# Optimization experiments

Measured on AMD Instinct MI355X. Metric: run time of the kernel, lower is better.

Reference implementation:

```python
import jax, jax.numpy as jnp
import numpy as np

INF = 1e10  # stand-in for +inf boundary of soft-DTW DP (safe under exp(-INF/gamma)=0)
HUBER_DELTA = 1.0
SDTW_ALPHA = 0.1
SDTW_GAMMA = 0.1


def _softmin3(a, b, c, gamma):
    # soft-min_gamma(a,b,c) = -gamma * logsumexp(-a/g, -b/g, -c/g)
    s = jnp.stack([a, b, c], axis=0) * (-1.0 / gamma)
    return -gamma * jax.nn.logsumexp(s, axis=0)


def _soft_dtw(x, y, gamma):
    # x, y: (B, L, C). Returns per-batch soft-DTW value R[L-1, L-1], shape (B,).
    B, L, C = x.shape
    # pairwise squared-euclidean distances (B, L, L) without (B,L,L,C) blowup
    x2 = jnp.sum(x * x, axis=-1)  # (B, L)
    y2 = jnp.sum(y * y, axis=-1)  # (B, L)
    D = x2[:, :, None] + y2[:, None, :] - 2.0 * jnp.einsum('blc,bmc->blm', x, y)

    i = jnp.arange(L)

    # Diagonals are stored as (B, L+1) arrays indexed by p = i + 1, so that the
    # virtual cell R[-1,-1] = 0 lives at p = 0 of diagonal k = -2.
    def step(carry, k):
        r2, r1 = carry  # diagonals k-2 and k-1
        j = k - i
        valid = (j >= 0) & (j < L)
        jc = jnp.clip(j, 0, L - 1)
        d = jnp.take_along_axis(D, jc[None, :, None], axis=2)[:, :, 0]  # (B, L) = D[:, i, k-i]
        a = r2[:, :-1]  # R[i-1, j-1]
        b = r1[:, :-1]  # R[i-1, j]
        c = r1[:, 1:]   # R[i, j-1]
        rk_vals = jnp.where(valid[None, :], d + _softmin3(a, b, c, gamma), INF)
        rk = jnp.concatenate([jnp.full((B, 1), INF, D.dtype), rk_vals], axis=1)
        return (r1, rk), None

    r2 = jnp.full((B, L + 1), INF, D.dtype).at[:, 0].set(0.0)  # diag k=-2: R[-1,-1]=0
    r1 = jnp.full((B, L + 1), INF, D.dtype)                    # diag k=-1: all inf
    (_, rlast), _ = jax.lax.scan(step, (r2, r1), jnp.arange(2 * L - 1))
    return rlast[:, L]  # R[L-1, L-1] per batch


def _huber_mean(x_hat, x, delta):
    d = x_hat - x
    ad = jnp.abs(d)
    loss = jnp.where(ad <= delta, 0.5 * d * d, delta * (ad - 0.5 * delta))
    return jnp.mean(loss)


def setup_inputs() -> dict:
    key = jax.random.key(0)
    k1, k2, k3 = jax.random.split(key, 3)
    B, L, C = 64, 512, 16
    x = jax.random.normal(k1, (B, L, C), dtype=jnp.float32)
    x_hat = jax.random.normal(k2, (B, L, C), dtype=jnp.float32)
    commitment_loss = jax.random.uniform(k3, (), dtype=jnp.float32)
    return {"x": x, "x_hat": x_hat, "commitment_loss": commitment_loss}


def reference(x, x_hat, commitment_loss):
    huber = _huber_mean(x_hat, x, HUBER_DELTA)
    sdtw = jnp.mean(_soft_dtw(x, x_hat, SDTW_GAMMA)) * SDTW_ALPHA
    total = huber + sdtw + commitment_loss
    # stacked [total, huber, sdtw, commitment] (torch module returns a dict of these scalars)
    return jnp.stack([total, huber, sdtw, commitment_loss])
```

## Files before the change

kernel.cpp:

```cpp
#include <hip/hip_runtime.h>
#include <math.h>


#define INFV 1.0e10f
static constexpr float kC1 = 14.4269504088896f;
static constexpr float kC2 = 0.0693147180559945f;

__device__ __forceinline__ int diag_off(int k) {
  if (k <= 512) return (k * (k + 1)) >> 1;
  int u = k - 512;
  return 131328 + 511 * u - ((u * (u - 1)) >> 1);
}
__device__ __forceinline__ int diag_i0(int k) { return k < 512 ? 0 : k - 511; }

__device__ __forceinline__ float huber1(float d) {
  float ad = fabsf(d);
  return ad <= 1.0f ? 0.5f * d * d : ad - 0.5f;
}

__global__ __launch_bounds__(256) void huber_kernel(const float* __restrict__ x,
                                                    const float* __restrict__ xh,
                                                    float* __restrict__ part) {
  int t = threadIdx.x;
  int gid = blockIdx.x * 256 + t;
  float s = 0.f;
  for (int i = gid; i < 131072; i += 65536) {
    float4 a = ((const float4*)x)[i];
    float4 b = ((const float4*)xh)[i];
    s += huber1(b.x - a.x) + huber1(b.y - a.y) + huber1(b.z - a.z) + huber1(b.w - a.w);
  }
  for (int o = 32; o > 0; o >>= 1) s += __shfl_down(s, o, 64);
  __shared__ float ws4[4];
  if ((t & 63) == 0) ws4[t >> 6] = s;
  __syncthreads();
  if (t == 0) part[blockIdx.x] = ws4[0] + ws4[1] + ws4[2] + ws4[3];
}

__global__ __launch_bounds__(256) void gemm_diag_kernel(const float* __restrict__ x,
                                                        const float* __restrict__ xh,
                                                        float* __restrict__ Dp) {
  const int b = blockIdx.z;
  const int ti = blockIdx.x;
  const int tj = blockIdx.y;
  const int t = threadIdx.x;
  __shared__ float sm[64 * 67];
  float* xsT = sm;
  float* ysT = sm + 16 * 68;
  const float* xb = x + ((size_t)b * 8192) + ti * 1024;
  const float* yb = xh + ((size_t)b * 8192) + tj * 1024;
  {
    float4 xv = ((const float4*)xb)[t];
    float4 yv = ((const float4*)yb)[t];
    int r = t >> 2, c0 = (t & 3) << 2;
    xsT[(c0 + 0) * 68 + r] = xv.x;
    xsT[(c0 + 1) * 68 + r] = xv.y;
    xsT[(c0 + 2) * 68 + r] = xv.z;
    xsT[(c0 + 3) * 68 + r] = xv.w;
    ysT[(c0 + 0) * 68 + r] = yv.x;
    ysT[(c0 + 1) * 68 + r] = yv.y;
    ysT[(c0 + 2) * 68 + r] = yv.z;
    ysT[(c0 + 3) * 68 + r] = yv.w;
  }
  __syncthreads();
  const int tm = t & 15, tn = t >> 4;
  float acc[4][4] = {};
  float y2a[4] = {};
#pragma unroll
  for (int c = 0; c < 16; ++c) {
    float4 xv = *(const float4*)&xsT[c * 68 + tm * 4];
    float4 yv = *(const float4*)&ysT[c * 68 + tn * 4];
    float xr[4] = {xv.x, xv.y, xv.z, xv.w};
    float yr[4] = {yv.x, yv.y, yv.z, yv.w};
#pragma unroll
    for (int n = 0; n < 4; ++n) {
      y2a[n] = fmaf(yr[n], yr[n], y2a[n]);
#pragma unroll
      for (int m = 0; m < 4; ++m) acc[m][n] = fmaf(xr[m], yr[n], acc[m][n]);
    }
  }
  __syncthreads();
#pragma unroll
  for (int m = 0; m < 4; ++m)
#pragma unroll
    for (int n = 0; n < 4; ++n)
      sm[(tm * 4 + m) * 67 + (tn * 4 + n)] = acc[m][n] - 0.5f * y2a[n];
  __syncthreads();
  const int lane = t & 63, wv = t >> 6;
  float* outb = Dp + (size_t)b * 262144;
  const int kbase = ti * 64 + tj * 64;
  for (int s = wv; s < 127; s += 4) {
    int ilo = s > 63 ? s - 63 : 0;
    int ihi = s < 63 ? s : 63;
    if (lane >= ilo && lane <= ihi) {
      float v = sm[lane * 67 + (s - lane)];
      int k = kbase + s;
      outb[diag_off(k) - diag_i0(k) + (ti * 64 + lane)] = v;
    }
  }
}

#define PSTEP(PN)                                                           \
  do {                                                                      \
    float bval = __shfl_up(vprev, 1);                                       \
    float rv = ringPrev[min(kk + 63, 574)];                                 \
    if (lane == 0) bval = (w == 0) ? INFV : rv;                             \
    float mv = fminf(fminf(aval, bval), vprev);                             \
    float md = __builtin_amdgcn_fmed3f(aval, bval, vprev);                  \
    float mx = fmaxf(fmaxf(aval, bval), vprev);                             \
    float ssum = 1.0f + exp2f((mv - md) * kC1) + exp2f((mv - mx) * kC1);    \
    float sm3 = fmaf(-kC2, log2f(ssum), mv);                                \
    float dotv = PN;                                                        \
    {                                                                       \
      int kc = k0 + min(kk + 10, 574);                                      \
      PN = DbL[diag_off(kc) - diag_i0(kc)];                                 \
    }                                                                       \
    float dd = fmaf(-2.0f, dotv, x2);                                       \
    float val = ((unsigned)(kk - lane) <= 511u) ? (dd + sm3) : INFV;        \
    if (lane == 63) ringOwn[kk] = val;                                      \
    aval = bval;                                                            \
    vprev = val;                                                            \
    ++kk;                                                                   \
  } while (0)

__global__ __launch_bounds__(512) void dtw_pipe_kernel(const float* __restrict__ x,
                                                       const float* __restrict__ Dp,
                                                       float* __restrict__ outv) {
  const int b = blockIdx.x;
  const int tid = threadIdx.x;
  const int w = tid >> 6;
  const int lane = tid & 63;
  __shared__ float ring[8][576];
  __shared__ int flags[8];
  if (tid < 8) flags[tid] = 0;
  __syncthreads();
  volatile int* vflags = flags;

  const int i = (w << 6) | lane;
  const float* xr = x + (size_t)b * 8192 + i * 16;
  float x2 = 0.f;
#pragma unroll
  for (int c = 0; c < 16; c += 4) {
    float4 v = *(const float4*)(xr + c);
    x2 += v.x * v.x + v.y * v.y + v.z * v.z + v.w * v.w;
  }
  const float* DbL = Dp + (size_t)b * 262144 + i;
  const int k0 = w << 6;

  float p[10];
#pragma unroll
  for (int n = 0; n < 10; ++n) {
    int kg = k0 + n;
    p[n] = DbL[diag_off(kg) - diag_i0(kg)];
  }

  float aval = (w == 0 && lane == 0) ? 0.0f : INFV;
  float vprev = INFV;
  float* ringOwn = ring[w];
  const float* ringPrev = ring[(w == 0) ? 7 : (w - 1)];

  int kk = 0;
#pragma unroll 1
  for (int ss = 0; ss < 58; ++ss) {
    const int nsub = (ss == 57) ? 5 : 10;
    if (w != 0) {
      const int need = min(kk + nsub + 63, 575);
      while (vflags[w - 1] < need) {
      }
      __threadfence_block();
    }
    if (nsub == 10) {
      PSTEP(p[0]); PSTEP(p[1]); PSTEP(p[2]); PSTEP(p[3]); PSTEP(p[4]);
      PSTEP(p[5]); PSTEP(p[6]); PSTEP(p[7]); PSTEP(p[8]); PSTEP(p[9]);
    } else {
      PSTEP(p[0]); PSTEP(p[1]); PSTEP(p[2]); PSTEP(p[3]); PSTEP(p[4]);
    }
    __threadfence_block();
    if (lane == 63) vflags[w] = kk;
  }
  if (tid == 511) outv[b] = vprev;
}

__device__ __forceinline__ float dot16(const float4& a, const float4& b2,
                                       const float4& c, const float4& d,
                                       const float4* yp) {
  float4 q0 = yp[0], q1 = yp[1], q2 = yp[2], q3 = yp[3];
  float s = a.x * q0.x;
  s = fmaf(a.y, q0.y, s); s = fmaf(a.z, q0.z, s); s = fmaf(a.w, q0.w, s);
  s = fmaf(b2.x, q1.x, s); s = fmaf(b2.y, q1.y, s); s = fmaf(b2.z, q1.z, s); s = fmaf(b2.w, q1.w, s);
  s = fmaf(c.x, q2.x, s); s = fmaf(c.y, q2.y, s); s = fmaf(c.w, q2.w, s); s = fmaf(c.z, q2.z, s);
  s = fmaf(d.x, q3.x, s); s = fmaf(d.y, q3.y, s); s = fmaf(d.z, q3.z, s); s = fmaf(d.w, q3.w, s);
  return s;
}

#define DTW_FSTEP(W, R1, R2)                                                \
  do {                                                                      \
    int j = k - tid;                                                        \
    bool valid = (j >= 0) && (j < 512);                                     \
    int jc = valid ? j : 0;                                                 \
    float av = R2[tid];                                                     \
    float bv = R1[tid];                                                     \
    float dotv = dot16(xa, xb4, xc4, xd4, (const float4*)&ysl[jc * 20]);    \
    float mv = fminf(fminf(av, bv), vprev);                                 \
    float ssum = exp2f((mv - av) * kC1) + exp2f((mv - bv) * kC1) +          \
                 exp2f((mv - vprev) * kC1);                                 \
    float sm3 = fmaf(-kC2, log2f(ssum), mv);                                \
    float dd = fmaf(-2.0f, dotv, x2 + y2s[jc]);                             \
    float val = valid ? (dd + sm3) : INFV;                                  \
    W[tid + 1] = val;                                                       \
    vprev = val;                                                            \
    __syncthreads();                                                        \
    ++k;                                                                    \
  } while (0)

__global__ __launch_bounds__(512) void dtw_fused_kernel(const float* __restrict__ x,
                                                        const float* __restrict__ xh,
                                                        float* __restrict__ outv) {
  const int b = blockIdx.x;
  const int tid = threadIdx.x;
  __shared__ float ysl[512 * 20];
  __shared__ float y2s[512];
  __shared__ float rA[516], rB[516], rC[516];
  const float* xr = x + (size_t)b * 8192 + tid * 16;
  const float* yr = xh + (size_t)b * 8192 + tid * 16;
  float4 xa = *(const float4*)(xr + 0);
  float4 xb4 = *(const float4*)(xr + 4);
  float4 xc4 = *(const float4*)(xr + 8);
  float4 xd4 = *(const float4*)(xr + 12);
  float x2 = xa.x * xa.x + xa.y * xa.y + xa.z * xa.z + xa.w * xa.w +
             xb4.x * xb4.x + xb4.y * xb4.y + xb4.z * xb4.z + xb4.w * xb4.w +
             xc4.x * xc4.x + xc4.y * xc4.y + xc4.z * xc4.z + xc4.w * xc4.w +
             xd4.x * xd4.x + xd4.y * xd4.y + xd4.z * xd4.z + xd4.w * xd4.w;
  {
    float4 q0 = *(const float4*)(yr + 0);
    float4 q1 = *(const float4*)(yr + 4);
    float4 q2 = *(const float4*)(yr + 8);
    float4 q3 = *(const float4*)(yr + 12);
    *(float4*)&ysl[tid * 20 + 0] = q0;
    *(float4*)&ysl[tid * 20 + 4] = q1;
    *(float4*)&ysl[tid * 20 + 8] = q2;
    *(float4*)&ysl[tid * 20 + 12] = q3;
    y2s[tid] = q0.x * q0.x + q0.y * q0.y + q0.z * q0.z + q0.w * q0.w +
               q1.x * q1.x + q1.y * q1.y + q1.z * q1.z + q1.w * q1.w +
               q2.x * q2.x + q2.y * q2.y + q2.z * q2.z + q2.w * q2.w +
               q3.x * q3.x + q3.y * q3.y + q3.z * q3.z + q3.w * q3.w;
  }
  rA[tid] = INFV;
  rB[tid] = INFV;
  rC[tid] = INFV;
  if (tid == 0) { rA[512] = INFV; rB[512] = INFV; rC[512] = INFV; }
  __syncthreads();
  float dot00 = dot16(xa, xb4, xc4, xd4, (const float4*)&ysl[0]);
  float d00 = fmaf(-2.0f, dot00, x2 + y2s[0]);
  float vprev = (tid == 0) ? d00 : INFV;
  if (tid == 0) rC[1] = d00;
  int k = 1;
  __syncthreads();
#pragma unroll 1
  for (int it = 0; it < 340; ++it) {
    DTW_FSTEP(rA, rC, rB);
    DTW_FSTEP(rB, rA, rC);
    DTW_FSTEP(rC, rB, rA);
  }
  DTW_FSTEP(rA, rC, rB);
  DTW_FSTEP(rB, rA, rC);
  if (tid == 511) outv[b] = vprev;
}

__global__ __launch_bounds__(256) void finalize_kernel(const float* __restrict__ part,
                                                       const float* __restrict__ dtwv,
                                                       const float* __restrict__ commit,
                                                       float* __restrict__ out) {
  int t = threadIdx.x;
  float h = part[t];
  float dv = (t < 64) ? dtwv[t] : 0.f;
  for (int o = 32; o > 0; o >>= 1) {
    h += __shfl_down(h, o, 64);
    dv += __shfl_down(dv, o, 64);
  }
  __shared__ float sh[4], sd[4];
  if ((t & 63) == 0) { sh[t >> 6] = h; sd[t >> 6] = dv; }
  __syncthreads();
  if (t == 0) {
    float hs = sh[0] + sh[1] + sh[2] + sh[3];
    float ds = sd[0] + sd[1] + sd[2] + sd[3];
    float hm = hs * (1.0f / 524288.0f);
    float smv = ds * (0.1f / 64.0f);
    float cm = commit[0];
    out[0] = hm + smv + cm;
    out[1] = hm;
    out[2] = smv;
    out[3] = cm;
  }
}

extern "C" void kernel_launch(void* const* d_in, const int* in_sizes, int n_in,
                              void* d_out, int out_size, void* d_ws, size_t ws_size,
                              hipStream_t stream) {
  (void)in_sizes; (void)n_in; (void)out_size;
  const float* x = (const float*)d_in[0];
  const float* xh = (const float*)d_in[1];
  const float* commit = (const float*)d_in[2];
  float* out = (float*)d_out;
  float* ws = (float*)d_ws;
  float* part = ws;
  float* dtwv = ws + 256;
  float* Dp = ws + 512;
  const size_t need = 2048 + (size_t)64 * 262144 * 4;

  huber_kernel<<<256, 256, 0, stream>>>(x, xh, part);
  if (ws_size >= need) {
    gemm_diag_kernel<<<dim3(8, 8, 64), 256, 0, stream>>>(x, xh, Dp);
    dtw_pipe_kernel<<<64, 512, 0, stream>>>(x, Dp, dtwv);
  } else {
    dtw_fused_kernel<<<64, 512, 0, stream>>>(x, xh, dtwv);
  }
  finalize_kernel<<<1, 256, 0, stream>>>(part, dtwv, commit, out);
}
```

Measured before the change: 353.0 us.

## Restructure soft-DTW wavefront pipeline with DPP shifts and double-buffered prefetch

The GEMM kernel now writes the full distance D (x2+y2-2xy) into the diagonal-packed buffer, so the DTW kernel no longer loads x or computes x2. The DTW pipeline replaces __shfl_up with DPP row-shift instructions, prefetches both D values and the ring values from the previous wave 8 steps ahead with A/B register double buffering, and syncs every 16 steps with a looser dependency window. Per-step fences are replaced by an lgkmcnt wait. The goal is to shorten the serial per-step latency on the critical path. The custom DPP handling at row boundaries and the relaxed memory fencing add correctness risk.

Measured after the change: 314.0 us. 1.12x faster.

```diff
diff --git a/kernel.cpp b/kernel.cpp
--- a/kernel.cpp
+++ b/kernel.cpp
@@ -12,6 +12,11 @@
   return 131328 + 511 * u - ((u * (u - 1)) >> 1);
 }
 __device__ __forceinline__ int diag_i0(int k) { return k < 512 ? 0 : k - 511; }
+__device__ __forceinline__ int fdiag(int k) {
+  if (k <= 511) return (k * (k + 1)) >> 1;
+  int u = k - 512;
+  return 131327 + 510 * u - ((u * (u - 1)) >> 1);
+}
 
 __device__ __forceinline__ float huber1(float d) {
   float ad = fabsf(d);
@@ -65,6 +70,7 @@
   const int tm = t & 15, tn = t >> 4;
   float acc[4][4] = {};
   float y2a[4] = {};
+  float x2a[4] = {};
 #pragma unroll
   for (int c = 0; c < 16; ++c) {
     float4 xv = *(const float4*)&xsT[c * 68 + tm * 4];
@@ -77,13 +83,15 @@
 #pragma unroll
       for (int m = 0; m < 4; ++m) acc[m][n] = fmaf(xr[m], yr[n], acc[m][n]);
     }
+#pragma unroll
+    for (int m = 0; m < 4; ++m) x2a[m] = fmaf(xr[m], xr[m], x2a[m]);
   }
   __syncthreads();
 #pragma unroll
   for (int m = 0; m < 4; ++m)
 #pragma unroll
     for (int n = 0; n < 4; ++n)
-      sm[(tm * 4 + m) * 67 + (tn * 4 + n)] = acc[m][n] - 0.5f * y2a[n];
+      sm[(tm * 4 + m) * 67 + (tn * 4 + n)] = fmaf(-2.0f, acc[m][n], x2a[m] + y2a[n]);
   __syncthreads();
   const int lane = t & 63, wv = t >> 6;
   float* outb = Dp + (size_t)b * 262144;
@@ -99,32 +107,37 @@
   }
 }
 
-#define PSTEP(PN)                                                           \
-  do {                                                                      \
-    float bval = __shfl_up(vprev, 1);                                       \
-    float rv = ringPrev[min(kk + 63, 574)];                                 \
-    if (lane == 0) bval = (w == 0) ? INFV : rv;                             \
-    float mv = fminf(fminf(aval, bval), vprev);                             \
-    float md = __builtin_amdgcn_fmed3f(aval, bval, vprev);                  \
-    float mx = fmaxf(fmaxf(aval, bval), vprev);                             \
-    float ssum = 1.0f + exp2f((mv - md) * kC1) + exp2f((mv - mx) * kC1);    \
-    float sm3 = fmaf(-kC2, log2f(ssum), mv);                                \
-    float dotv = PN;                                                        \
-    {                                                                       \
-      int kc = k0 + min(kk + 10, 574);                                      \
-      PN = DbL[diag_off(kc) - diag_i0(kc)];                                 \
-    }                                                                       \
-    float dd = fmaf(-2.0f, dotv, x2);                                       \
-    float val = ((unsigned)(kk - lane) <= 511u) ? (dd + sm3) : INFV;        \
-    if (lane == 63) ringOwn[kk] = val;                                      \
-    aval = bval;                                                            \
-    vprev = val;                                                            \
-    ++kk;                                                                   \
+#define PSTEP(PC, RC, PN, RN)                                                          \
+  do {                                                                                 \
+    {                                                                                  \
+      int kc = kk + 8; kc = kc > 575 ? 575 : kc;                                       \
+      int kg = k0 + kc;                                                                \
+      PN = DbL[fdiag(kg)];                                                             \
+      int ri = kc + 63; ri = ri > 574 ? 574 : ri;                                      \
+      RN = ringPrev[ri];                                                               \
+    }                                                                                  \
+    int vi = __float_as_int(vprev);                                                    \
+    float bs = __int_as_float(__builtin_amdgcn_update_dpp(0, vi, 0x111, 0xF, 0xF, true)); \
+    float bb = __int_as_float(__builtin_amdgcn_update_dpp(0, vi, 0x142, 0xF, 0xF, true)); \
+    float bval = fixl ? bb : bs;                                                       \
+    float l0v = w ? RC : INFV;                                                         \
+    bval = isl0 ? l0v : bval;                                                          \
+    float mv = fminf(fminf(aval, bval), vprev);                                        \
+    float md = __builtin_amdgcn_fmed3f(aval, bval, vprev);                             \
+    float mx = fmaxf(fmaxf(aval, bval), vprev);                                        \
+    float e1 = exp2f((mv - md) * kC1);                                                 \
+    float e2 = exp2f((mv - mx) * kC1);                                                 \
+    float lg = log2f(1.0f + e1 + e2);                                                  \
+    float d_eff = ((unsigned)(kk - lane) <= 511u) ? PC : INFV;                         \
+    float val = fmaf(-kC2, lg, mv + d_eff);                                            \
+    if (lane == 63) ringOwn[kk] = val;                                                 \
+    aval = bval;                                                                       \
+    vprev = val;                                                                       \
+    ++kk;                                                                              \
   } while (0)
 
-__global__ __launch_bounds__(512) void dtw_pipe_kernel(const float* __restrict__ x,
-                                                       const float* __restrict__ Dp,
-                                                       float* __restrict__ outv) {
+__global__ __launch_bounds__(512) void dtw_pipe2_kernel(const float* __restrict__ Dp,
+                                                        float* __restrict__ outv) {
   const int b = blockIdx.x;
   const int tid = threadIdx.x;
   const int w = tid >> 6;
@@ -135,49 +148,56 @@
   __syncthreads();
   volatile int* vflags = flags;
 
-  const int i = (w << 6) | lane;
-  const float* xr = x + (size_t)b * 8192 + i * 16;
-  float x2 = 0.f;
-#pragma unroll
-  for (int c = 0; c < 16; c += 4) {
-    float4 v = *(const float4*)(xr + c);
-    x2 += v.x * v.x + v.y * v.y + v.z * v.z + v.w * v.w;
-  }
-  const float* DbL = Dp + (size_t)b * 262144 + i;
+  const bool isl0 = (lane == 0);
+  const bool fixl = ((lane & 15) == 0) && (lane != 0);
+  const float* DbL = Dp + (size_t)b * 262144 + tid;
   const int k0 = w << 6;
-
-  float p[10];
-#pragma unroll
-  for (int n = 0; n < 10; ++n) {
-    int kg = k0 + n;
-    p[n] = DbL[diag_off(kg) - diag_i0(kg)];
-  }
-
-  float aval = (w == 0 && lane == 0) ? 0.0f : INFV;
+  float* ringOwn = ring[w];
+  const float* ringPrev = ring[(w + 7) & 7];
+
+  if (w) {
+    while (vflags[w - 1] < 71) {}
+  }
+  asm volatile("" ::: "memory");
+
+  float pA[8], pB[8], rA[8], rB[8];
+#pragma unroll
+  for (int j = 0; j < 8; ++j) {
+    pA[j] = DbL[fdiag(k0 + j)];
+    rA[j] = ringPrev[63 + j];
+  }
+  float aval = (tid == 0) ? 0.0f : INFV;
   float vprev = INFV;
-  float* ringOwn = ring[w];
-  const float* ringPrev = ring[(w == 0) ? 7 : (w - 1)];
-
   int kk = 0;
+
 #pragma unroll 1
-  for (int ss = 0; ss < 58; ++ss) {
-    const int nsub = (ss == 57) ? 5 : 10;
-    if (w != 0) {
-      const int need = min(kk + nsub + 63, 575);
-      while (vflags[w - 1] < need) {
-      }
-      __threadfence_block();
+  for (int it = 0; it < 36; ++it) {
+    if (w) {
+      int need = kk + 87;
+      need = need > 575 ? 575 : need;
+      while (vflags[w - 1] < need) {}
     }
-    if (nsub == 10) {
-      PSTEP(p[0]); PSTEP(p[1]); PSTEP(p[2]); PSTEP(p[3]); PSTEP(p[4]);
-      PSTEP(p[5]); PSTEP(p[6]); PSTEP(p[7]); PSTEP(p[8]); PSTEP(p[9]);
-    } else {
-      PSTEP(p[0]); PSTEP(p[1]); PSTEP(p[2]); PSTEP(p[3]); PSTEP(p[4]);
-    }
-    __threadfence_block();
+    asm volatile("" ::: "memory");
+    PSTEP(pA[0], rA[0], pB[0], rB[0]);
+    PSTEP(pA[1], rA[1], pB[1], rB[1]);
+    PSTEP(pA[2], rA[2], pB[2], rB[2]);
+    PSTEP(pA[3], rA[3], pB[3], rB[3]);
+    PSTEP(pA[4], rA[4], pB[4], rB[4]);
+    PSTEP(pA[5], rA[5], pB[5], rB[5]);
+    PSTEP(pA[6], rA[6], pB[6], rB[6]);
+    PSTEP(pA[7], rA[7], pB[7], rB[7]);
+    PSTEP(pB[0], rB[0], pA[0], rA[0]);
+    PSTEP(pB[1], rB[1], pA[1], rA[1]);
+    PSTEP(pB[2], rB[2], pA[2], rA[2]);
+    PSTEP(pB[3], rB[3], pA[3], rA[3]);
+    PSTEP(pB[4], rB[4], pA[4], rA[4]);
+    PSTEP(pB[5], rB[5], pA[5], rA[5]);
+    PSTEP(pB[6], rB[6], pA[6], rA[6]);
+    PSTEP(pB[7], rB[7], pA[7], rA[7]);
+    asm volatile("s_waitcnt lgkmcnt(0)" ::: "memory");
     if (lane == 63) vflags[w] = kk;
   }
-  if (tid == 511) outv[b] = vprev;
+  if (tid == 511) outv[b] = ringOwn[574];
 }
 
 __device__ __forceinline__ float dot16(const float4& a, const float4& b2,
@@ -187,7 +207,7 @@
   float s = a.x * q0.x;
   s = fmaf(a.y, q0.y, s); s = fmaf(a.z, q0.z, s); s = fmaf(a.w, q0.w, s);
   s = fmaf(b2.x, q1.x, s); s = fmaf(b2.y, q1.y, s); s = fmaf(b2.z, q1.z, s); s = fmaf(b2.w, q1.w, s);
-  s = fmaf(c.x, q2.x, s); s = fmaf(c.y, q2.y, s); s = fmaf(c.w, q2.w, s); s = fmaf(c.z, q2.z, s);
+  s = fmaf(c.x, q2.x, s); s = fmaf(c.y, q2.y, s); s = fmaf(c.z, q2.z, s); s = fmaf(c.w, q2.w, s);
   s = fmaf(d.x, q3.x, s); s = fmaf(d.y, q3.y, s); s = fmaf(d.z, q3.z, s); s = fmaf(d.w, q3.w, s);
   return s;
 }
@@ -206,7 +226,7 @@
     float sm3 = fmaf(-kC2, log2f(ssum), mv);                                \
     float dd = fmaf(-2.0f, dotv, x2 + y2s[jc]);                             \
     float val = valid ? (dd + sm3) : INFV;                                  \
-    W[tid + 1] = val;                                                       \
+    W[tid + 1] = val;                                                      \
     vprev = val;                                                            \
     __syncthreads();                                                        \
     ++k;                                                                    \
@@ -310,7 +330,7 @@
   huber_kernel<<<256, 256, 0, stream>>>(x, xh, part);
   if (ws_size >= need) {
     gemm_diag_kernel<<<dim3(8, 8, 64), 256, 0, stream>>>(x, xh, Dp);
-    dtw_pipe_kernel<<<64, 512, 0, stream>>>(x, Dp, dtwv);
+    dtw_pipe2_kernel<<<64, 512, 0, stream>>>(Dp, dtwv);
   } else {
     dtw_fused_kernel<<<64, 512, 0, stream>>>(x, xh, dtwv);
   }
```
